# Kernel optimization log

Hardware: AMD Instinct MI355X
Metric: run time of the kernel (lower is better)

The kernel has to match this reference:

```python
import jax, jax.numpy as jnp
import numpy as np

N = 100000   # nodes
E = 1600000  # edges (avg degree 16)
IN, HID, OUT = 128, 128, 40


def setup_inputs() -> dict:
    key = jax.random.key(0)
    ks = jax.random.split(key, 7)
    return {
        "features": jax.random.normal(ks[0], (N, IN), jnp.float32),
        "src": jax.random.randint(ks[1], (E,), 0, N, jnp.int32),
        "dst": jax.random.randint(ks[2], (E,), 0, N, jnp.int32),
        "W1": jax.random.normal(ks[3], (IN, HID), jnp.float32) / np.sqrt(IN).astype(np.float32),
        "Wh": jax.random.normal(ks[4], (HID, HID), jnp.float32) / np.sqrt(HID).astype(np.float32),
        "W2": jax.random.normal(ks[5], (HID, OUT), jnp.float32) / np.sqrt(HID).astype(np.float32),
        "b2": jnp.zeros((OUT,), jnp.float32),
    }


def _agg(x, src, dst):
    # message passing: gather source node features along edges, sum-scatter to dst
    return jax.ops.segment_sum(x[src], dst, num_segments=N)


def reference(features, src, dst, W1, Wh, W2, b2):
    ones = jnp.ones((E,), jnp.float32)
    out_deg = jnp.clip(jax.ops.segment_sum(ones, src, num_segments=N), 1.0)
    in_deg = jnp.clip(jax.ops.segment_sum(ones, dst, num_segments=N), 1.0)
    lnorm = out_deg[:, None] ** -0.5  # 'both' left norm (src out-degree)
    rnorm = in_deg[:, None] ** -0.5   # 'both' right norm (dst in-degree)

    # conv1: GraphConv(norm='none', bias=False) -> plain sum aggregation, then relu
    h = jax.nn.relu(_agg(features @ W1, src, dst))
    # hidden GraphConv(norm='both', bias=False) + relu (dropout = identity in eval)
    h = jax.nn.relu(_agg((h * lnorm) @ Wh, src, dst) * rnorm)
    # conv2: GraphConv(norm='both', bias=True)
    h = _agg((h * lnorm) @ W2, src, dst) * rnorm + b2
    return jax.nn.log_softmax(h, axis=1)
```

## Files before the change

kernel.cpp:

```cpp
#include <hip/hip_runtime.h>
#include <math.h>

#define MAXDEG 64
#define BCAP 8192
#define EPB 4096

typedef __attribute__((ext_vector_type(8))) short bf16x8;
typedef __attribute__((ext_vector_type(4))) float f32x4;

static __device__ inline unsigned short f2bf(float f) {
    unsigned int u = __float_as_uint(f);
    u += 0x7FFFu + ((u >> 16) & 1u);
    return (unsigned short)(u >> 16);
}
static __device__ inline float bf2f(unsigned short u) {
    return __uint_as_float(((unsigned int)u) << 16);
}
static __device__ inline float4 ld_f4(const float* p) { return *(const float4*)p; }

static __device__ __forceinline__ void accu16(float* a, uint4 u, float f) {
    a[0]  += f * (float)(u.x & 0xffu);
    a[1]  += f * (float)((u.x >> 8) & 0xffu);
    a[2]  += f * (float)((u.x >> 16) & 0xffu);
    a[3]  += f * (float)(u.x >> 24);
    a[4]  += f * (float)(u.y & 0xffu);
    a[5]  += f * (float)((u.y >> 8) & 0xffu);
    a[6]  += f * (float)((u.y >> 16) & 0xffu);
    a[7]  += f * (float)(u.y >> 24);
    a[8]  += f * (float)(u.z & 0xffu);
    a[9]  += f * (float)((u.z >> 8) & 0xffu);
    a[10] += f * (float)((u.z >> 16) & 0xffu);
    a[11] += f * (float)(u.z >> 24);
    a[12] += f * (float)(u.w & 0xffu);
    a[13] += f * (float)((u.w >> 8) & 0xffu);
    a[14] += f * (float)((u.w >> 16) & 0xffu);
    a[15] += f * (float)(u.w >> 24);
}

static __global__ __launch_bounds__(256) void wtrans_kernel(
    const float* __restrict__ W1, const float* __restrict__ Wh,
    const float* __restrict__ W2,
    unsigned short* __restrict__ W1t, unsigned short* __restrict__ WhT,
    unsigned short* __restrict__ Wt2) {
    int b = blockIdx.x;
    int t = threadIdx.x;
    if (b == 2) {
        for (int i = t; i < 48 * 128; i += 256) Wt2[i] = 0;
        __syncthreads();
        int n0 = (t & 31) * 4;
        if (n0 < 40) {
            for (int k = t >> 5; k < 128; k += 8) {
                float4 v = ld_f4(&W2[(size_t)k * 40 + n0]);
                Wt2[(size_t)(n0 + 0) * 128 + k] = f2bf(v.x);
                Wt2[(size_t)(n0 + 1) * 128 + k] = f2bf(v.y);
                Wt2[(size_t)(n0 + 2) * 128 + k] = f2bf(v.z);
                Wt2[(size_t)(n0 + 3) * 128 + k] = f2bf(v.w);
            }
        }
        return;
    }
    const float* Wsrc = (b == 0) ? W1 : Wh;
    unsigned short* Wdst = (b == 0) ? W1t : WhT;
    int n0 = (t & 31) * 4;
    for (int k = t >> 5; k < 128; k += 8) {
        float4 v = ld_f4(&Wsrc[(size_t)k * 128 + n0]);
        Wdst[(size_t)(n0 + 0) * 128 + k] = f2bf(v.x);
        Wdst[(size_t)(n0 + 1) * 128 + k] = f2bf(v.y);
        Wdst[(size_t)(n0 + 2) * 128 + k] = f2bf(v.z);
        Wdst[(size_t)(n0 + 3) * 128 + k] = f2bf(v.w);
    }
}

static __device__ __forceinline__ void gemm128_mfma256_q(
    const unsigned short* sa16, const unsigned short* __restrict__ Wt,
    unsigned char* __restrict__ Y, float* __restrict__ sc,
    int row0, int t, int N) {
    int l = t & 63, w = t >> 6;
    int m = l & 15, kg = l >> 4;
    int row = w * 16 + m;
    int rsw = row & 15;
    f32x4 acc[8];
#pragma unroll
    for (int c = 0; c < 8; ++c) acc[c] = (f32x4){0.f, 0.f, 0.f, 0.f};
#pragma unroll
    for (int ks = 0; ks < 4; ++ks) {
        bf16x8 a = *(const bf16x8*)&sa16[(size_t)row * 128 + (((ks * 4 + kg) ^ rsw) * 8)];
        int kk = ks * 32 + kg * 8;
#pragma unroll
        for (int c = 0; c < 8; ++c) {
            bf16x8 b = *(const bf16x8*)&Wt[(size_t)(c * 16 + m) * 128 + kk];
            acc[c] = __builtin_amdgcn_mfma_f32_16x16x32_bf16(a, b, acc[c], 0, 0, 0);
        }
    }
#pragma unroll
    for (int r = 0; r < 4; ++r) {
        float lm = 0.f;
#pragma unroll
        for (int c = 0; c < 8; ++c) lm = fmaxf(lm, fabsf(acc[c][r]));
#pragma unroll
        for (int o = 1; o < 16; o <<= 1) lm = fmaxf(lm, __shfl_xor(lm, o));
        float inv = lm > 0.f ? 127.f / lm : 0.f;
        int grow = row0 + w * 16 + kg * 4 + r;
        if (grow < N) {
#pragma unroll
            for (int c = 0; c < 8; ++c)
                Y[(size_t)grow * 128 + c * 16 + m] =
                    (unsigned char)(__float2int_rn(acc[c][r] * inv) + 128);
            if (m == 0) sc[grow] = lm * (1.f / 127.f);
        }
    }
}

static __device__ __forceinline__ void gemm128_mfma512_q(
    const unsigned short* sa16, const unsigned short* __restrict__ Wt,
    unsigned char* __restrict__ Y, float* __restrict__ sc,
    unsigned* rmaxu, int row0, int t, int N) {
    int l = t & 63, w = t >> 6;
    int rt = w >> 1, ctb = (w & 1) * 4;
    int m = l & 15, kg = l >> 4;
    int row = rt * 16 + m;
    int rsw = row & 15;
    f32x4 acc[4] = {{0.f, 0.f, 0.f, 0.f}, {0.f, 0.f, 0.f, 0.f},
                    {0.f, 0.f, 0.f, 0.f}, {0.f, 0.f, 0.f, 0.f}};
#pragma unroll
    for (int ks = 0; ks < 4; ++ks) {
        bf16x8 a = *(const bf16x8*)&sa16[(size_t)row * 128 + (((ks * 4 + kg) ^ rsw) * 8)];
        int kk = ks * 32 + kg * 8;
#pragma unroll
        for (int c = 0; c < 4; ++c) {
            int n = (ctb + c) * 16 + m;
            bf16x8 b = *(const bf16x8*)&Wt[(size_t)n * 128 + kk];
            acc[c] = __builtin_amdgcn_mfma_f32_16x16x32_bf16(a, b, acc[c], 0, 0, 0);
        }
    }
#pragma unroll
    for (int r = 0; r < 4; ++r) {
        float lm = 0.f;
#pragma unroll
        for (int c = 0; c < 4; ++c) lm = fmaxf(lm, fabsf(acc[c][r]));
#pragma unroll
        for (int o = 1; o < 16; o <<= 1) lm = fmaxf(lm, __shfl_xor(lm, o));
        if (m == 0)
            atomicMax(&rmaxu[rt * 16 + kg * 4 + r], __float_as_uint(lm));
    }
    __syncthreads();
#pragma unroll
    for (int r = 0; r < 4; ++r) {
        int rl = rt * 16 + kg * 4 + r;
        float am = __uint_as_float(rmaxu[rl]);
        float inv = am > 0.f ? 127.f / am : 0.f;
        int grow = row0 + rl;
        if (grow < N) {
#pragma unroll
            for (int c = 0; c < 4; ++c)
                Y[(size_t)grow * 128 + (ctb + c) * 16 + m] =
                    (unsigned char)(__float2int_rn(acc[c][r] * inv) + 128);
            if (ctb == 0 && m == 0) sc[grow] = am * (1.f / 127.f);
        }
    }
}

static __device__ __forceinline__ void gemm40_mfma512(
    const unsigned short* sa16, const unsigned short* __restrict__ Wt2,
    unsigned short* __restrict__ Y3, int row0, int t, int N) {
    int l = t & 63, w = t >> 6;
    int rt = w & 3;
    int nct = (w < 4) ? 2 : 1;
    int ct0 = (w < 4) ? 0 : 2;
    int m = l & 15, kg = l >> 4;
    int row = rt * 16 + m;
    int rsw = row & 15;
    f32x4 acc[2] = {{0.f, 0.f, 0.f, 0.f}, {0.f, 0.f, 0.f, 0.f}};
#pragma unroll
    for (int ks = 0; ks < 4; ++ks) {
        bf16x8 a = *(const bf16x8*)&sa16[(size_t)row * 128 + (((ks * 4 + kg) ^ rsw) * 8)];
        int kk = ks * 32 + kg * 8;
        for (int c = 0; c < nct; ++c) {
            int n = (ct0 + c) * 16 + m;
            bf16x8 b = *(const bf16x8*)&Wt2[(size_t)n * 128 + kk];
            acc[c] = __builtin_amdgcn_mfma_f32_16x16x32_bf16(a, b, acc[c], 0, 0, 0);
        }
    }
    for (int c = 0; c < nct; ++c) {
        int col = (ct0 + c) * 16 + m;
        if (col >= 40) continue;
#pragma unroll
        for (int r = 0; r < 4; ++r) {
            int grow = row0 + rt * 16 + kg * 4 + r;
            if (grow < N) Y3[(size_t)grow * 40 + col] = f2bf(acc[c][r]);
        }
    }
}

template <int MODE>
static __device__ __forceinline__ void gather_phase_u8(
    const unsigned char* __restrict__ Ysrc, const float* __restrict__ scs,
    unsigned short* sa16,
    const int* __restrict__ csr, const int* __restrict__ indeg,
    const int* __restrict__ outdeg, int row0, int t, int N) {
    int w = t >> 6;
    int l = t & 63;
    int q = l >> 4;
    int lq = l & 15;
    int qb = q * 16;
    int oct = lq >> 3;
    int ol = lq & 7;

#pragma unroll
    for (int i = 0; i < 2; ++i) {
        int r = i * 32 + w * 4 + q;
        int node = row0 + r;
        bool valid = node < N;
        int d = 0;
        if (valid) d = indeg[node];
        int dc = d > MAXDEG ? MAXDEG : d;

        int idx0 = 0, idx1 = 0, idx2 = 0, idx3 = 0;
        float sc0 = 0.f, sc1 = 0.f, sc2 = 0.f, sc3 = 0.f;
        if (valid) {
            const int* cp = csr + (size_t)node * MAXDEG;
            if (lq < dc)      { idx0 = cp[lq];      sc0 = scs[idx0]; }
            if (lq + 16 < dc) { idx1 = cp[lq + 16]; sc1 = scs[idx1]; }
            if (lq + 32 < dc) { idx2 = cp[lq + 32]; sc2 = scs[idx2]; }
            if (lq + 48 < dc) { idx3 = cp[lq + 48]; sc3 = scs[idx3]; }
        }

        float a[16];
#pragma unroll
        for (int x = 0; x < 16; ++x) a[x] = 0.f;
        float S = 0.f;

#pragma unroll
        for (int c = 0; c < 4; ++c) {
            int ebase = c * 16;
            if (ebase >= dc) break;
            int v = (c == 0) ? idx0 : (c == 1) ? idx1 : (c == 2) ? idx2 : idx3;
            float vs = (c == 0) ? sc0 : (c == 1) ? sc1 : (c == 2) ? sc2 : sc3;
            int lim = dc - ebase;
            if (lim > 16) lim = 16;
            for (int e = 0; e < lim; e += 2) {
                int s = __shfl(v, qb + e + oct);
                float f = __shfl(vs, qb + e + oct);
                uint4 u = *(const uint4*)&Ysrc[(size_t)s * 128 + ol * 16];
                S += f;
                accu16(a, u, f);
            }
        }

#pragma unroll
        for (int x = 0; x < 16; ++x) a[x] += __shfl_xor(a[x], 8);
        S += __shfl_xor(S, 8);

        if (valid) {
            float bias = 128.f * S;
            int od = outdeg[node];
            float ln = rsqrtf((float)(od > 1 ? od : 1));
            if (MODE == 0) {
#pragma unroll
                for (int x = 0; x < 16; ++x)
                    a[x] = fmaxf(a[x] - bias, 0.f) * ln;
            } else {
                float rn = rsqrtf((float)(d > 1 ? d : 1));
#pragma unroll
                for (int x = 0; x < 16; ++x)
                    a[x] = fmaxf((a[x] - bias) * rn, 0.f) * ln;
            }
        } else {
#pragma unroll
            for (int x = 0; x < 16; ++x) a[x] = 0.f;
        }

        uint4 uo;
        if (oct == 0) {
            uo.x = (unsigned)f2bf(a[0]) | ((unsigned)f2bf(a[1]) << 16);
            uo.y = (unsigned)f2bf(a[2]) | ((unsigned)f2bf(a[3]) << 16);
            uo.z = (unsigned)f2bf(a[4]) | ((unsigned)f2bf(a[5]) << 16);
            uo.w = (unsigned)f2bf(a[6]) | ((unsigned)f2bf(a[7]) << 16);
        } else {
            uo.x = (unsigned)f2bf(a[8]) | ((unsigned)f2bf(a[9]) << 16);
            uo.y = (unsigned)f2bf(a[10]) | ((unsigned)f2bf(a[11]) << 16);
            uo.z = (unsigned)f2bf(a[12]) | ((unsigned)f2bf(a[13]) << 16);
            uo.w = (unsigned)f2bf(a[14]) | ((unsigned)f2bf(a[15]) << 16);
        }
        int chunk = (2 * ol + oct) ^ (r & 15);
        *(uint4*)&sa16[(size_t)r * 128 + chunk * 8] = uo;
    }
}

static __global__ __launch_bounds__(256) void bucket_gemm1_kernel(
    const float* __restrict__ A, const unsigned short* __restrict__ W1t,
    unsigned char* __restrict__ Y, float* __restrict__ s1,
    const int* __restrict__ src, const int* __restrict__ dst,
    int* __restrict__ cntD, int* __restrict__ cntS,
    unsigned int* __restrict__ bktD, unsigned char* __restrict__ bktS,
    int N, int E, int nb, int gG, int gB) {
    __shared__ unsigned short sa16[64 * 128];
    int bid = blockIdx.x;
    int t = threadIdx.x;

    int nI = 5 * gB;
    int role, idx;
    if (bid < nI) {
        if (bid % 5 == 0) { role = 1; idx = bid / 5; }
        else { role = 0; idx = bid - bid / 5 - 1; }
    } else { role = 0; idx = bid - gB; }
    if (role == 1 && idx >= gB) return;
    if (role == 0 && idx >= gG) return;

    if (role == 1) {
        int* sh = (int*)sa16;
        int* hD = sh;
        int* hS = sh + 512;
        int* bD = sh + 1024;
        int* bS = sh + 1536;
        int* cD = sh + 2048;
        int* cS = sh + 2560;
        for (int i = t; i < 512; i += 256) {
            hD[i] = 0; hS[i] = 0; cD[i] = 0; cS[i] = 0;
        }
        __syncthreads();

        int base = idx * EPB + t * 16;
        int s_r[16], d_r[16];
        int nv = 0;
        if (base + 16 <= E) {
            nv = 16;
#pragma unroll
            for (int k = 0; k < 4; ++k) {
                int4 sv = *(const int4*)&src[base + k * 4];
                int4 dv = *(const int4*)&dst[base + k * 4];
                s_r[k * 4 + 0] = sv.x; s_r[k * 4 + 1] = sv.y;
                s_r[k * 4 + 2] = sv.z; s_r[k * 4 + 3] = sv.w;
                d_r[k * 4 + 0] = dv.x; d_r[k * 4 + 1] = dv.y;
                d_r[k * 4 + 2] = dv.z; d_r[k * 4 + 3] = dv.w;
            }
        } else {
            nv = E - base; if (nv < 0) nv = 0; if (nv > 16) nv = 16;
#pragma unroll
            for (int k = 0; k < 16; ++k) {
                if (k < nv) { s_r[k] = src[base + k]; d_r[k] = dst[base + k]; }
                else { s_r[k] = 0; d_r[k] = 0; }
            }
        }

#pragma unroll
        for (int k = 0; k < 16; ++k) {
            if (k < nv) {
                atomicAdd(&hD[d_r[k] >> 8], 1);
                atomicAdd(&hS[s_r[k] >> 8], 1);
            }
        }
        __syncthreads();

        for (int b = t; b < nb; b += 256) {
            int h = hD[b];
            bD[b] = h ? atomicAdd(&cntD[b], h) : 0;
            int h2 = hS[b];
            bS[b] = h2 ? atomicAdd(&cntS[b], h2) : 0;
        }
        __syncthreads();

#pragma unroll
        for (int k = 0; k < 16; ++k) {
            if (k < nv) {
                int d = d_r[k], s = s_r[k];
                int bb = d >> 8;
                int p = atomicAdd(&cD[bb], 1) + bD[bb];
                if (p < BCAP)
                    bktD[(size_t)bb * BCAP + p] =
                        ((unsigned int)(d & 255) << 17) | (unsigned int)s;
                int sb = s >> 8;
                int p2 = atomicAdd(&cS[sb], 1) + bS[sb];
                if (p2 < BCAP)
                    bktS[(size_t)sb * BCAP + p2] = (unsigned char)(s & 255);
            }
        }
        return;
    }

    int row0 = idx * 64;
#pragma unroll
    for (int i = 0; i < 4; ++i) {
        int ci = i * 256 + t;
        int r = ci >> 4;
        int ch = ci & 15;
        int grow = row0 + r;
        uint4 uo = make_uint4(0u, 0u, 0u, 0u);
        if (grow < N) {
            float4 v0 = ld_f4(&A[(size_t)grow * 128 + ch * 8]);
            float4 v1 = ld_f4(&A[(size_t)grow * 128 + ch * 8 + 4]);
            uo.x = (unsigned)f2bf(v0.x) | ((unsigned)f2bf(v0.y) << 16);
            uo.y = (unsigned)f2bf(v0.z) | ((unsigned)f2bf(v0.w) << 16);
            uo.z = (unsigned)f2bf(v1.x) | ((unsigned)f2bf(v1.y) << 16);
            uo.w = (unsigned)f2bf(v1.z) | ((unsigned)f2bf(v1.w) << 16);
        }
        int chunk = ch ^ (r & 15);
        *(uint4*)&sa16[(size_t)r * 128 + chunk * 8] = uo;
    }
    __syncthreads();
    gemm128_mfma256_q(sa16, W1t, Y, s1, row0, t, N);
}

static __global__ __launch_bounds__(256) void csr_build_kernel(
    const int* __restrict__ cntD, const int* __restrict__ cntS,
    const unsigned int* __restrict__ bktD, const unsigned char* __restrict__ bktS,
    int* __restrict__ csr, int* __restrict__ indeg, int* __restrict__ outdeg,
    int N, int nb) {
    __shared__ int cur[256];
    int bid = blockIdx.x;
    int t = threadIdx.x;
    cur[t] = 0;
    __syncthreads();

    if (bid < nb) {
        int b = bid;
        int cnt = cntD[b]; if (cnt > BCAP) cnt = BCAP;
        const unsigned int* bp = bktD + (size_t)b * BCAP;
        for (int i = t; i < cnt; i += 256) {
            unsigned int v = bp[i];
            int d8 = v >> 17;
            int s = (int)(v & 0x1FFFFu);
            int p = atomicAdd(&cur[d8], 1);
            if (p < MAXDEG) csr[((size_t)(b * 256 + d8)) * MAXDEG + p] = s;
        }
        __syncthreads();
        int node = b * 256 + t;
        if (node < N) indeg[node] = cur[t];
    } else {
        int b = bid - nb;
        int cnt = cntS[b]; if (cnt > BCAP) cnt = BCAP;
        const unsigned char* bp = bktS + (size_t)b * BCAP;
        for (int i = t; i < cnt; i += 256) atomicAdd(&cur[bp[i]], 1);
        __syncthreads();
        int node = b * 256 + t;
        if (node < N) outdeg[node] = cur[t];
    }
}

static __global__ __launch_bounds__(512) void agg_gemm2_kernel(
    const unsigned char* __restrict__ Y1, const float* __restrict__ s1,
    const unsigned short* __restrict__ WhT,
    unsigned char* __restrict__ Y2, float* __restrict__ s2,
    const int* __restrict__ csr, const int* __restrict__ indeg,
    const int* __restrict__ outdeg, int N) {
    __shared__ unsigned short sa16[64 * 128];
    __shared__ unsigned rmaxu[64];
    int t = threadIdx.x;
    if (t < 64) rmaxu[t] = 0u;
    int row0 = blockIdx.x * 64;
    gather_phase_u8<0>(Y1, s1, sa16, csr, indeg, outdeg, row0, t, N);
    __syncthreads();
    gemm128_mfma512_q(sa16, WhT, Y2, s2, rmaxu, row0, t, N);
}

static __global__ __launch_bounds__(512) void agg_gemm3_kernel(
    const unsigned char* __restrict__ Y2, const float* __restrict__ s2,
    const unsigned short* __restrict__ Wt2,
    unsigned short* __restrict__ Y3,
    const int* __restrict__ csr, const int* __restrict__ indeg,
    const int* __restrict__ outdeg, int N) {
    __shared__ unsigned short sa16[64 * 128];
    int t = threadIdx.x;
    int row0 = blockIdx.x * 64;
    gather_phase_u8<1>(Y2, s2, sa16, csr, indeg, outdeg, row0, t, N);
    __syncthreads();
    gemm40_mfma512(sa16, Wt2, Y3, row0, t, N);
}

static __global__ __launch_bounds__(512) void agg40_lsm_kernel(
    const unsigned short* __restrict__ Y3, const float* __restrict__ b2,
    const int* __restrict__ csr, const int* __restrict__ indeg,
    float* __restrict__ out, int N) {
    int t = threadIdx.x;
    int node = blockIdx.x * 8 + (t >> 6);
    if (node >= N) return;
    int lane = t & 63;
    int grp = lane >> 4;
    int sub = lane & 15;
    int d = indeg[node];
    int dc = d > MAXDEG ? MAXDEG : d;

    float a0 = 0.f, a1 = 0.f, a2 = 0.f, a3 = 0.f;
    if (sub < 10) {
        const int* cp = csr + (size_t)node * MAXDEG;
        int e = grp;
        for (; e + 12 < dc; e += 16) {
            int s0 = cp[e];
            int s1 = cp[e + 4];
            int s2 = cp[e + 8];
            int s3 = cp[e + 12];
            ushort4 u0 = *(const ushort4*)&Y3[(size_t)s0 * 40 + sub * 4];
            ushort4 u1 = *(const ushort4*)&Y3[(size_t)s1 * 40 + sub * 4];
            ushort4 u2 = *(const ushort4*)&Y3[(size_t)s2 * 40 + sub * 4];
            ushort4 u3 = *(const ushort4*)&Y3[(size_t)s3 * 40 + sub * 4];
            a0 += bf2f(u0.x) + bf2f(u1.x) + bf2f(u2.x) + bf2f(u3.x);
            a1 += bf2f(u0.y) + bf2f(u1.y) + bf2f(u2.y) + bf2f(u3.y);
            a2 += bf2f(u0.z) + bf2f(u1.z) + bf2f(u2.z) + bf2f(u3.z);
            a3 += bf2f(u0.w) + bf2f(u1.w) + bf2f(u2.w) + bf2f(u3.w);
        }
        for (; e < dc; e += 4) {
            int s = cp[e];
            ushort4 u = *(const ushort4*)&Y3[(size_t)s * 40 + sub * 4];
            a0 += bf2f(u.x); a1 += bf2f(u.y); a2 += bf2f(u.z); a3 += bf2f(u.w);
        }
    }
    a0 += __shfl_xor(a0, 16); a0 += __shfl_xor(a0, 32);
    a1 += __shfl_xor(a1, 16); a1 += __shfl_xor(a1, 32);
    a2 += __shfl_xor(a2, 16); a2 += __shfl_xor(a2, 32);
    a3 += __shfl_xor(a3, 16); a3 += __shfl_xor(a3, 32);

    float rs = rsqrtf((float)(d > 1 ? d : 1));
    float x0 = 0.f, x1 = 0.f, x2 = 0.f, x3 = 0.f;
    float mx = -INFINITY;
    if (sub < 10) {
        float4 b = *(const float4*)&b2[sub * 4];
        x0 = a0 * rs + b.x;
        x1 = a1 * rs + b.y;
        x2 = a2 * rs + b.z;
        x3 = a3 * rs + b.w;
        mx = fmaxf(fmaxf(x0, x1), fmaxf(x2, x3));
    }
#pragma unroll
    for (int o = 1; o < 16; o <<= 1) mx = fmaxf(mx, __shfl_xor(mx, o));
    float ex = 0.f;
    if (sub < 10)
        ex = expf(x0 - mx) + expf(x1 - mx) + expf(x2 - mx) + expf(x3 - mx);
#pragma unroll
    for (int o = 1; o < 16; o <<= 1) ex += __shfl_xor(ex, o);
    float ls = logf(ex) + mx;
    if (sub < 10 && grp == 0)
        *(float4*)&out[(size_t)node * 40 + sub * 4] =
            make_float4(x0 - ls, x1 - ls, x2 - ls, x3 - ls);
}


extern "C" void kernel_launch(void* const* d_in, const int* in_sizes, int n_in,
                              void* d_out, int out_size, void* d_ws, size_t ws_size,
                              hipStream_t stream) {
    const float* features = (const float*)d_in[0];
    const int* src = (const int*)d_in[1];
    const int* dst = (const int*)d_in[2];
    const float* W1 = (const float*)d_in[3];
    const float* Wh = (const float*)d_in[4];
    const float* W2 = (const float*)d_in[5];
    const float* b2 = (const float*)d_in[6];
    float* out = (float*)d_out;

    const int N = in_sizes[0] / 128;
    const int E = in_sizes[1];
    const int nb = (N + 255) / 256;

    char* p = (char*)d_ws;
    auto carve = [&](size_t bytes) {
        char* q = p;
        p += (bytes + 255) & ~(size_t)255;
        return q;
    };
    unsigned char* bufY1 = (unsigned char*)carve((size_t)N * 128);
    float* sc1 = (float*)carve((size_t)N * 4);
    unsigned char* bufY2 = (unsigned char*)carve((size_t)N * 128);
    float* sc2 = (float*)carve((size_t)N * 4);
    unsigned short* bufY3 = (unsigned short*)carve((size_t)N * 40 * 2);
    int* csr = (int*)carve((size_t)N * MAXDEG * 4);
    unsigned int* bktD = (unsigned int*)carve((size_t)nb * BCAP * 4);
    unsigned char* bktS = (unsigned char*)carve((size_t)nb * BCAP);
    int* cntD = (int*)carve((size_t)nb * 4);
    int* cntS = (int*)carve((size_t)nb * 4);
    int* indeg = (int*)carve((size_t)N * 4);
    int* outdeg = (int*)carve((size_t)N * 4);
    unsigned short* W1t = (unsigned short*)carve((size_t)128 * 128 * 2);
    unsigned short* WhT = (unsigned short*)carve((size_t)128 * 128 * 2);
    unsigned short* Wt2 = (unsigned short*)carve((size_t)48 * 128 * 2);
    (void)ws_size; (void)n_in; (void)out_size;

    hipMemsetAsync(cntD, 0, (size_t)nb * 4, stream);
    hipMemsetAsync(cntS, 0, (size_t)nb * 4, stream);

    int gG = (N + 63) / 64;
    int gB = (E + EPB - 1) / EPB;
    wtrans_kernel<<<3, 256, 0, stream>>>(W1, Wh, W2, W1t, WhT, Wt2);
    bucket_gemm1_kernel<<<gG + gB, 256, 0, stream>>>(
        features, W1t, bufY1, sc1, src, dst, cntD, cntS, bktD, bktS,
        N, E, nb, gG, gB);
    csr_build_kernel<<<2 * nb, 256, 0, stream>>>(
        cntD, cntS, bktD, bktS, csr, indeg, outdeg, N, nb);
    agg_gemm2_kernel<<<gG, 512, 0, stream>>>(bufY1, sc1, WhT, bufY2, sc2,
                                             csr, indeg, outdeg, N);
    agg_gemm3_kernel<<<gG, 512, 0, stream>>>(bufY2, sc2, Wt2, bufY3,
                                             csr, indeg, outdeg, N);
    agg40_lsm_kernel<<<(N + 7) / 8, 512, 0, stream>>>(bufY3, b2, csr, indeg, out, N);
}
```

Baseline: 287.0 us.

## Remap gather to 8 lanes per node with 4-way unrolled neighbor loads

The gather phase now assigns one node to each group of 8 lanes, with every lane covering a 16-byte slice of the 128-byte row. Before, 16 lanes handled a node, split into two octets that each took alternate edges, and the two partial sums were merged with cross-lane shuffles. This drops the shuffle reduction and the two-iteration loop over row groups. The inner edge loop is unrolled by four so several independent row loads are in flight at once. Each lane now walks every edge serially and holds more index registers, and edges past 32 fall back to a scalar path that reads the CSR directly.

```diff
diff --git a/kernel.cpp b/kernel.cpp
--- a/kernel.cpp
+++ b/kernel.cpp
@@ -200,91 +200,108 @@
     const int* __restrict__ outdeg, int row0, int t, int N) {
     int w = t >> 6;
     int l = t & 63;
-    int q = l >> 4;
-    int lq = l & 15;
-    int qb = q * 16;
-    int oct = lq >> 3;
-    int ol = lq & 7;
-
-#pragma unroll
-    for (int i = 0; i < 2; ++i) {
-        int r = i * 32 + w * 4 + q;
-        int node = row0 + r;
-        bool valid = node < N;
-        int d = 0;
-        if (valid) d = indeg[node];
-        int dc = d > MAXDEG ? MAXDEG : d;
-
-        int idx0 = 0, idx1 = 0, idx2 = 0, idx3 = 0;
-        float sc0 = 0.f, sc1 = 0.f, sc2 = 0.f, sc3 = 0.f;
-        if (valid) {
-            const int* cp = csr + (size_t)node * MAXDEG;
-            if (lq < dc)      { idx0 = cp[lq];      sc0 = scs[idx0]; }
-            if (lq + 16 < dc) { idx1 = cp[lq + 16]; sc1 = scs[idx1]; }
-            if (lq + 32 < dc) { idx2 = cp[lq + 32]; sc2 = scs[idx2]; }
-            if (lq + 48 < dc) { idx3 = cp[lq + 48]; sc3 = scs[idx3]; }
-        }
-
-        float a[16];
+    int g8 = l >> 3;
+    int le = l & 7;
+    int gb = g8 * 8;
+
+    int r = w * 8 + g8;
+    int node = row0 + r;
+    bool valid = node < N;
+    int d = 0;
+    if (valid) d = indeg[node];
+    int dc = d > MAXDEG ? MAXDEG : d;
+    int dc32 = dc > 32 ? 32 : dc;
+
+    const int* cp = csr + (size_t)node * MAXDEG;
+    int idx0 = 0, idx1 = 0, idx2 = 0, idx3 = 0;
+    float sv0 = 0.f, sv1 = 0.f, sv2 = 0.f, sv3 = 0.f;
+    if (valid) {
+        if (le < dc32)      { idx0 = cp[le];      sv0 = scs[idx0]; }
+        if (le + 8 < dc32)  { idx1 = cp[le + 8];  sv1 = scs[idx1]; }
+        if (le + 16 < dc32) { idx2 = cp[le + 16]; sv2 = scs[idx2]; }
+        if (le + 24 < dc32) { idx3 = cp[le + 24]; sv3 = scs[idx3]; }
+    }
+
+    float a[16];
+#pragma unroll
+    for (int x = 0; x < 16; ++x) a[x] = 0.f;
+    float S = 0.f;
+
+#pragma unroll
+    for (int c = 0; c < 4; ++c) {
+        int ebase = c * 8;
+        if (ebase >= dc32) break;
+        int v = (c == 0) ? idx0 : (c == 1) ? idx1 : (c == 2) ? idx2 : idx3;
+        float vs = (c == 0) ? sv0 : (c == 1) ? sv1 : (c == 2) ? sv2 : sv3;
+        int lim = dc32 - ebase;
+        if (lim > 8) lim = 8;
+        int e = 0;
+        for (; e + 4 <= lim; e += 4) {
+            int s0 = __shfl(v, gb + e);
+            int s1 = __shfl(v, gb + e + 1);
+            int s2 = __shfl(v, gb + e + 2);
+            int s3 = __shfl(v, gb + e + 3);
+            float f0 = __shfl(vs, gb + e);
+            float f1 = __shfl(vs, gb + e + 1);
+            float f2 = __shfl(vs, gb + e + 2);
+            float f3 = __shfl(vs, gb + e + 3);
+            uint4 u0 = *(const uint4*)&Ysrc[(size_t)s0 * 128 + le * 16];
+            uint4 u1 = *(const uint4*)&Ysrc[(size_t)s1 * 128 + le * 16];
+            uint4 u2 = *(const uint4*)&Ysrc[(size_t)s2 * 128 + le * 16];
+            uint4 u3 = *(const uint4*)&Ysrc[(size_t)s3 * 128 + le * 16];
+            S += f0 + f1 + f2 + f3;
+            accu16(a, u0, f0); accu16(a, u1, f1);
+            accu16(a, u2, f2); accu16(a, u3, f3);
+        }
+        for (; e < lim; ++e) {
+            int s0 = __shfl(v, gb + e);
+            float f0 = __shfl(vs, gb + e);
+            uint4 u0 = *(const uint4*)&Ysrc[(size_t)s0 * 128 + le * 16];
+            S += f0;
+            accu16(a, u0, f0);
+        }
+    }
+    if (valid) {
+        for (int e = 32; e < dc; ++e) {
+            int s = cp[e];
+            float f = scs[s];
+            uint4 u = *(const uint4*)&Ysrc[(size_t)s * 128 + le * 16];
+            S += f;
+            accu16(a, u, f);
+        }
+    }
+
+    if (valid) {
+        float bias = 128.f * S;
+        int od = outdeg[node];
+        float ln = rsqrtf((float)(od > 1 ? od : 1));
+        if (MODE == 0) {
+#pragma unroll
+            for (int x = 0; x < 16; ++x)
+                a[x] = fmaxf(a[x] - bias, 0.f) * ln;
+        } else {
+            float rn = rsqrtf((float)(d > 1 ? d : 1));
+#pragma unroll
+            for (int x = 0; x < 16; ++x)
+                a[x] = fmaxf((a[x] - bias) * rn, 0.f) * ln;
+        }
+    } else {
 #pragma unroll
         for (int x = 0; x < 16; ++x) a[x] = 0.f;
-        float S = 0.f;
-
-#pragma unroll
-        for (int c = 0; c < 4; ++c) {
-            int ebase = c * 16;
-            if (ebase >= dc) break;
-            int v = (c == 0) ? idx0 : (c == 1) ? idx1 : (c == 2) ? idx2 : idx3;
-            float vs = (c == 0) ? sc0 : (c == 1) ? sc1 : (c == 2) ? sc2 : sc3;
-            int lim = dc - ebase;
-            if (lim > 16) lim = 16;
-            for (int e = 0; e < lim; e += 2) {
-                int s = __shfl(v, qb + e + oct);
-                float f = __shfl(vs, qb + e + oct);
-                uint4 u = *(const uint4*)&Ysrc[(size_t)s * 128 + ol * 16];
-                S += f;
-                accu16(a, u, f);
-            }
-        }
-
-#pragma unroll
-        for (int x = 0; x < 16; ++x) a[x] += __shfl_xor(a[x], 8);
-        S += __shfl_xor(S, 8);
-
-        if (valid) {
-            float bias = 128.f * S;
-            int od = outdeg[node];
-            float ln = rsqrtf((float)(od > 1 ? od : 1));
-            if (MODE == 0) {
-#pragma unroll
-                for (int x = 0; x < 16; ++x)
-                    a[x] = fmaxf(a[x] - bias, 0.f) * ln;
-            } else {
-                float rn = rsqrtf((float)(d > 1 ? d : 1));
-#pragma unroll
-                for (int x = 0; x < 16; ++x)
-                    a[x] = fmaxf((a[x] - bias) * rn, 0.f) * ln;
-            }
-        } else {
-#pragma unroll
-            for (int x = 0; x < 16; ++x) a[x] = 0.f;
-        }
-
-        uint4 uo;
-        if (oct == 0) {
-            uo.x = (unsigned)f2bf(a[0]) | ((unsigned)f2bf(a[1]) << 16);
-            uo.y = (unsigned)f2bf(a[2]) | ((unsigned)f2bf(a[3]) << 16);
-            uo.z = (unsigned)f2bf(a[4]) | ((unsigned)f2bf(a[5]) << 16);
-            uo.w = (unsigned)f2bf(a[6]) | ((unsigned)f2bf(a[7]) << 16);
-        } else {
-            uo.x = (unsigned)f2bf(a[8]) | ((unsigned)f2bf(a[9]) << 16);
-            uo.y = (unsigned)f2bf(a[10]) | ((unsigned)f2bf(a[11]) << 16);
-            uo.z = (unsigned)f2bf(a[12]) | ((unsigned)f2bf(a[13]) << 16);
-            uo.w = (unsigned)f2bf(a[14]) | ((unsigned)f2bf(a[15]) << 16);
-        }
-        int chunk = (2 * ol + oct) ^ (r & 15);
-        *(uint4*)&sa16[(size_t)r * 128 + chunk * 8] = uo;
-    }
+    }
+
+    int rsw = r & 15;
+    uint4 uo0, uo1;
+    uo0.x = (unsigned)f2bf(a[0]) | ((unsigned)f2bf(a[1]) << 16);
+    uo0.y = (unsigned)f2bf(a[2]) | ((unsigned)f2bf(a[3]) << 16);
+    uo0.z = (unsigned)f2bf(a[4]) | ((unsigned)f2bf(a[5]) << 16);
+    uo0.w = (unsigned)f2bf(a[6]) | ((unsigned)f2bf(a[7]) << 16);
+    uo1.x = (unsigned)f2bf(a[8]) | ((unsigned)f2bf(a[9]) << 16);
+    uo1.y = (unsigned)f2bf(a[10]) | ((unsigned)f2bf(a[11]) << 16);
+    uo1.z = (unsigned)f2bf(a[12]) | ((unsigned)f2bf(a[13]) << 16);
+    uo1.w = (unsigned)f2bf(a[14]) | ((unsigned)f2bf(a[15]) << 16);
+    *(uint4*)&sa16[(size_t)r * 128 + ((2 * le) ^ rsw) * 8] = uo0;
+    *(uint4*)&sa16[(size_t)r * 128 + ((2 * le + 1) ^ rsw) * 8] = uo1;
 }
 
 static __global__ __launch_bounds__(256) void bucket_gemm1_kernel(
```

After: 281.2 us. 1.02x faster.
